# Optimization experiments

Measured on AMD Instinct MI355X. Metric: run time of the kernel, lower is better.

The kernel has to match this reference:

```python
import jax, jax.numpy as jnp
import numpy as np


def _bce_logits(x, z):
    # numerically stable binary_cross_entropy_with_logits (elementwise)
    return jnp.maximum(x, 0.0) - x * z + jnp.log1p(jnp.exp(-jnp.abs(x)))


def _giou(b1, b2):
    # boxes in (cx, cy, w, h) format, mirrors bbox_iou(..., mode='giou')
    eps = 1e-9
    b1x1 = b1[..., 0] - b1[..., 2] / 2; b1y1 = b1[..., 1] - b1[..., 3] / 2
    b1x2 = b1[..., 0] + b1[..., 2] / 2; b1y2 = b1[..., 1] + b1[..., 3] / 2
    b2x1 = b2[..., 0] - b2[..., 2] / 2; b2y1 = b2[..., 1] - b2[..., 3] / 2
    b2x2 = b2[..., 0] + b2[..., 2] / 2; b2y2 = b2[..., 1] + b2[..., 3] / 2
    a1 = jnp.clip(b1x2 - b1x1, 0.0) * jnp.clip(b1y2 - b1y1, 0.0) + eps
    a2 = jnp.clip(b2x2 - b2x1, 0.0) * jnp.clip(b2y2 - b2y1, 0.0) + eps
    iw = jnp.clip(jnp.minimum(b1x2, b2x2) - jnp.maximum(b1x1, b2x1), 0.0)
    ih = jnp.clip(jnp.minimum(b1y2, b2y2) - jnp.maximum(b1y1, b2y1), 0.0)
    inter = iw * ih + eps
    union = a1 + a2 - inter + eps
    iou = inter / union
    cw = jnp.maximum(b1x2, b2x2) - jnp.minimum(b1x1, b2x1)
    ch = jnp.maximum(b1y2, b2y2) - jnp.minimum(b1y1, b2y1)
    carea = cw * ch + eps
    return iou - (carea - union) / carea


def setup_inputs() -> dict:
    key = jax.random.key(0)
    ks = jax.random.split(key, 8)
    N, A, S, nC, nM, G, H, W = 4, 3, 13, 80, 32, 16, 104, 104
    preds = jax.random.normal(ks[0], (N, A, S, S, 5 + nC + nM), jnp.float32) * 0.5
    prototypes = jax.random.normal(ks[1], (N, nM, H, W), jnp.float32)
    masks = (jax.random.uniform(ks[2], (N, G, H, W)) < 0.3).astype(jnp.float32)
    ii = jnp.arange(S)
    interior = (ii >= 2) & (ii <= 10)
    int2d = interior[:, None] & interior[None, :]
    obj = (jax.random.uniform(ks[3], (N, A, S, S)) < 0.06) & int2d
    obj = obj.at[:, 0, 6, 6].set(True)  # guarantee >= 1 object per image
    xy = jax.random.uniform(ks[4], (N, A, S, S, 2), minval=0.2, maxval=0.8)
    wh = jax.random.uniform(ks[5], (N, A, S, S, 2), minval=0.5, maxval=2.5)
    cls = jax.random.randint(ks[6], (N, A, S, S, 1), 0, nC).astype(jnp.float32)
    mid = jax.random.randint(ks[7], (N, A, S, S, 1), 0, G).astype(jnp.float32)
    target = jnp.concatenate([xy, wh, obj[..., None].astype(jnp.float32), cls, mid], axis=-1)
    anchors = jnp.array([[1.0, 1.5], [2.0, 2.5], [3.5, 3.0]], jnp.float32)
    return {"preds": preds, "target": target, "anchors": anchors,
            "prototypes": prototypes, "masks": masks,
            "num_classes": 80, "num_masks": 32}


def reference(preds, target, anchors, prototypes, masks, num_classes, num_masks):
    eps = 1e-9
    N, A, S = preds.shape[0], preds.shape[1], preds.shape[2]
    H, W = prototypes.shape[2], prototypes.shape[3]
    nC, nM = num_classes, num_masks
    dt = preds.dtype
    conf_t = target[..., 4]
    obj = conf_t == 1.0
    noobj = conf_t == 0.0
    objf = obj.astype(dt)
    noobjf = noobj.astype(dt)
    n_obj = objf.sum()
    n_noobj = noobjf.sum()
    conf_logit = preds[..., 4]
    noobj_loss = (_bce_logits(conf_logit, conf_t) * noobjf).sum() / n_noobj
    # ---- segmentation loss (dense masked equivalent of ragged per-instance crops) ----
    coeffs = jnp.tanh(preds[..., 5 + nC:5 + nC + nM])            # [N,A,S,S,M]
    inst = jnp.einsum('naijm,nmhw->naijhw', coeffs, prototypes)   # instance logits
    cols = jnp.arange(S, dtype=dt)
    # cells_to_boxes: normalized image coords, then scaled to prototype pixels
    bx = (target[..., 0] + cols[None, None, None, :]) / S * W
    by = (target[..., 1] + cols[None, None, :, None]) / S * H
    bw = target[..., 2] / S * W
    bh = target[..., 3] / S * H
    x1 = jnp.floor(bx - bw / 2).astype(jnp.int32)
    x2 = jnp.floor(bx + bw / 2).astype(jnp.int32)
    y1 = jnp.floor(by - bh / 2).astype(jnp.int32)
    y2 = jnp.floor(by + bh / 2).astype(jnp.int32)
    ids = jnp.clip(target[..., 6].astype(jnp.int32), 0, masks.shape[1] - 1)
    tm = masks[jnp.arange(N)[:, None, None, None], ids]           # [N,A,S,S,H,W]
    hh = jnp.arange(H)
    ww = jnp.arange(W)
    rm = ((hh >= y1[..., None]) & (hh < y2[..., None])).astype(dt)  # [N,A,S,S,H]
    cm = ((ww >= x1[..., None]) & (ww < x2[..., None])).astype(dt)  # [N,A,S,S,W]
    bce_el = _bce_logits(inst, tm)
    region_sum = jnp.einsum('naijhw,naijh,naijw->naij', bce_el, rm, cm)
    area = rm.sum(-1) * cm.sum(-1)
    valid = (area > 0) & obj
    seg_mean = jnp.where(valid, region_sum / jnp.maximum(area, 1.0), 0.0)
    segment_loss = seg_mean.sum() / (valid.astype(dt).sum() + eps)
    # ---- box / obj / class losses ----
    anch = anchors.reshape(1, A, 1, 1, 2)
    pred_box = jnp.concatenate([jax.nn.sigmoid(preds[..., 0:2]),
                                jnp.exp(preds[..., 2:4]) * anch], axis=-1)
    giou = _giou(pred_box, target[..., 0:4])                      # [N,A,S,S]
    obj_tgt = conf_t * jnp.clip(jax.lax.stop_gradient(giou), 0.0)
    obj_loss = (_bce_logits(conf_logit, obj_tgt) * objf).sum() / n_obj
    # note: original applies BCEWithLogits to sigmoid(xy) (double squash) - faithful
    xy_bce = (_bce_logits(jax.nn.sigmoid(preds[..., 0:2]), target[..., 0:2])
              * objf[..., None]).sum() / (n_obj * 2)
    twh = jnp.log(1e-16 + target[..., 2:4] / anch)
    wh_mse = (((preds[..., 2:4] - twh) ** 2) * objf[..., None]).sum() / (n_obj * 2)
    box_loss = xy_bce + wh_mse + ((1.0 - giou) * objf).sum() / n_obj
    logp = jax.nn.log_softmax(preds[..., 5:5 + nC], axis=-1)
    labels = target[..., 5].astype(jnp.int32)
    nll = -jnp.take_along_axis(logp, labels[..., None], axis=-1)[..., 0]
    class_loss = (nll * objf).sum() / n_obj
    box_l = 8.0 * box_loss
    obj_l = 2.0 * obj_loss
    noobj_l = 4.0 * noobj_loss
    cls_l = 1.0 * class_loss
    seg_l = 10.0 * segment_loss
    total = box_l + obj_l + noobj_l + cls_l + seg_l
    return jnp.stack([box_l, obj_l, noobj_l, cls_l, seg_l, total])
```

## Files before the change

### kernel.cpp

```cpp
#include <hip/hip_runtime.h>
#include <math.h>

#define N_  4
#define A_  3
#define S_  13
#define NC_ 80
#define NM_ 32
#define G_  16
#define H_  104
#define W_  104
#define CH_ (5 + NC_ + NM_)
#define HW_ (H_ * W_)
#define NCELL (N_ * A_ * S_ * S_)

#define MAIN_BLOCKS 64
#define PROW 16

__device__ __forceinline__ float bce_logits(float x, float z) {
    return fmaxf(x, 0.0f) - x * z + log1pf(expf(-fabsf(x)));
}

__device__ __forceinline__ float sigmoidf(float x) {
    return 1.0f / (1.0f + expf(-x));
}

__device__ __forceinline__ float readlane_f(float v, int l) {
    return __int_as_float(__builtin_amdgcn_readlane(__float_as_int(v), l));
}

__device__ __forceinline__ float giou_fn(float cx1, float cy1, float w1, float h1,
                                         float cx2, float cy2, float w2, float h2) {
    const float eps = 1e-9f;
    float b1x1 = cx1 - w1 * 0.5f, b1y1 = cy1 - h1 * 0.5f;
    float b1x2 = cx1 + w1 * 0.5f, b1y2 = cy1 + h1 * 0.5f;
    float b2x1 = cx2 - w2 * 0.5f, b2y1 = cy2 - h2 * 0.5f;
    float b2x2 = cx2 + w2 * 0.5f, b2y2 = cy2 + h2 * 0.5f;
    float a1 = fmaxf(b1x2 - b1x1, 0.0f) * fmaxf(b1y2 - b1y1, 0.0f) + eps;
    float a2 = fmaxf(b2x2 - b2x1, 0.0f) * fmaxf(b2y2 - b2y1, 0.0f) + eps;
    float iw = fmaxf(fminf(b1x2, b2x2) - fmaxf(b1x1, b2x1), 0.0f);
    float ih = fmaxf(fminf(b1y2, b2y2) - fmaxf(b1y1, b2y1), 0.0f);
    float inter = iw * ih + eps;
    float uni   = a1 + a2 - inter + eps;
    float iou   = inter / uni;
    float cw = fmaxf(b1x2, b2x2) - fminf(b1x1, b2x1);
    float ch = fmaxf(b1y2, b2y2) - fminf(b1y1, b2y1);
    float carea = cw * ch + eps;
    return iou - (carea - uni) / carea;
}

__device__ __forceinline__ int region_bounds(const float* t, int i, int j,
                                             int& lox, int& loy, int& ncols, int& nrows) {
    float bx = (t[0] + (float)j) * ((float)W_ / (float)S_);
    float by = (t[1] + (float)i) * ((float)H_ / (float)S_);
    float bw = t[2] * ((float)W_ / (float)S_);
    float bh = t[3] * ((float)H_ / (float)S_);
    int x1 = (int)floorf(bx - bw * 0.5f);
    int x2 = (int)floorf(bx + bw * 0.5f);
    int y1 = (int)floorf(by - bh * 0.5f);
    int y2 = (int)floorf(by + bh * 0.5f);
    lox = max(x1, 0); loy = max(y1, 0);
    ncols = max(min(x2, W_) - lox, 0);
    nrows = max(min(y2, H_) - loy, 0);
    return nrows * ncols;
}

__global__ __launch_bounds__(256) void yolo_fused_kernel(
    const float* __restrict__ preds,
    const float* __restrict__ target,
    const float* __restrict__ anchors,
    const float* __restrict__ protos,
    const float* __restrict__ masks,
    float* __restrict__ partials,
    unsigned int* __restrict__ ticket,
    float* __restrict__ out)
{
    const int b    = blockIdx.x;
    const int tid  = threadIdx.x;
    const int wav  = tid >> 6;
    const int lane = tid & 63;

    __shared__ float s_w[4][8];
    __shared__ float s_red[4];
    __shared__ int   s_list[40];
    __shared__ int   s_nvalid;
    __shared__ int   s_last;

    if (b < 8) {
        const int cell = b * 256 + tid;
        float v0 = 0.f, v1 = 0.f, v2 = 0.f, v3 = 0.f,
              v4 = 0.f, v5 = 0.f, v6 = 0.f, v7 = 0.f;

        if (cell < NCELL) {
            const int a = (cell / (S_ * S_)) % A_;
            const float* t = target + (size_t)cell * 7;
            const float* p = preds  + (size_t)cell * CH_;
            const float conf_t = t[4];
            const float x = p[4];

            if (conf_t == 0.0f) {
                v1 = 1.0f;
                v2 = bce_logits(x, 0.0f);
            } else if (conf_t == 1.0f) {
                v0 = 1.0f;
                float tx = t[0], ty = t[1], tw = t[2], th = t[3];
                float aw = anchors[a * 2 + 0], ah = anchors[a * 2 + 1];
                float sx = sigmoidf(p[0]);
                float sy = sigmoidf(p[1]);
                float pw = expf(p[2]) * aw;
                float ph = expf(p[3]) * ah;
                float giou = giou_fn(sx, sy, pw, ph, tx, ty, tw, th);
                v3 = bce_logits(x, fmaxf(giou, 0.0f));
                v4 = bce_logits(sx, tx) + bce_logits(sy, ty);
                float twl = logf(1e-16f + tw / aw);
                float thl = logf(1e-16f + th / ah);
                float dw = p[2] - twl, dh = p[3] - thl;
                v5 = dw * dw + dh * dh;
                v6 = 1.0f - giou;

                float mx = -1e30f;
                #pragma unroll 8
                for (int c = 0; c < NC_; ++c) mx = fmaxf(mx, p[5 + c]);
                float se = 0.0f;
                #pragma unroll 8
                for (int c = 0; c < NC_; ++c) se += expf(p[5 + c] - mx);
                int label = (int)t[5];
                v7 = (mx + logf(se)) - p[5 + label];
            }
        }

        #pragma unroll
        for (int o = 32; o > 0; o >>= 1) {
            v0 += __shfl_xor(v0, o, 64);  v1 += __shfl_xor(v1, o, 64);
            v2 += __shfl_xor(v2, o, 64);  v3 += __shfl_xor(v3, o, 64);
            v4 += __shfl_xor(v4, o, 64);  v5 += __shfl_xor(v5, o, 64);
            v6 += __shfl_xor(v6, o, 64);  v7 += __shfl_xor(v7, o, 64);
        }
        if ((tid & 63) == 0) {
            int w = tid >> 6;
            s_w[w][0] = v0; s_w[w][1] = v1; s_w[w][2] = v2; s_w[w][3] = v3;
            s_w[w][4] = v4; s_w[w][5] = v5; s_w[w][6] = v6; s_w[w][7] = v7;
        }
        __syncthreads();
        if (tid < 8) {
            partials[b * PROW + tid] =
                s_w[0][tid] + s_w[1][tid] + s_w[2][tid] + s_w[3][tid];
        }
    }

    if (tid == 0) s_nvalid = 0;
    __syncthreads();
    if (tid < 32) {
        int c = tid * 64 + b;
        if (c < NCELL) {
            const float* t = target + (size_t)c * 7;
            if (t[4] == 1.0f) {
                int lox, loy, ncols, nrows;
                int area = region_bounds(t, (c / S_) % S_, c % S_,
                                         lox, loy, ncols, nrows);
                if (area > 0) {
                    int k = atomicAdd(&s_nvalid, 1);
                    s_list[k] = c;
                }
            }
        }
    }
    __syncthreads();
    const int nv = s_nvalid;

    float wave_seg = 0.0f;
    for (int ii = wav; ii < nv; ii += 4) {
        const int cell = s_list[ii];
        const int j = cell % S_;
        const int i = (cell / S_) % S_;
        const int n = cell / (A_ * S_ * S_);
        const float* t = target + (size_t)cell * 7;
        const float* p = preds  + (size_t)cell * CH_;

        int lox, loy, ncols, nrows;
        region_bounds(t, i, j, lox, loy, ncols, nrows);
        const int area = nrows * ncols;

        float cv = 0.0f;
        if (lane < NM_) cv = tanhf(p[5 + NC_ + lane]);
        float cm[NM_];
        #pragma unroll
        for (int m = 0; m < NM_; ++m) cm[m] = readlane_f(cv, m);

        int id = (int)t[6];
        id = min(max(id, 0), G_ - 1);
        const float* tm = masks  + ((size_t)(n * G_ + id)) * HW_;
        const float* pr = protos + (size_t)n * NM_ * HW_;

        float lsum = 0.0f;
        for (int px = lane; px < area; px += 64) {
            int h = loy + px / ncols;
            int w = lox + px % ncols;
            int off = h * W_ + w;
            float inst = 0.0f;
            #pragma unroll
            for (int m = 0; m < NM_; ++m)
                inst += cm[m] * pr[m * HW_ + off];
            lsum += bce_logits(inst, tm[off]);
        }

        #pragma unroll
        for (int o = 32; o > 0; o >>= 1) lsum += __shfl_xor(lsum, o, 64);
        if (lane == 0) wave_seg += lsum / fmaxf((float)area, 1.0f);
    }

    if (lane == 0) s_red[wav] = wave_seg;
    __syncthreads();
    if (tid == 0) {
        partials[b * PROW + 8] = s_red[0] + s_red[1] + s_red[2] + s_red[3];
        partials[b * PROW + 9] = (float)nv;
    }

    __threadfence();
    __syncthreads();
    if (tid == 0) {
        unsigned int old = atomicInc(ticket, MAIN_BLOCKS - 1u);
        s_last = (old == MAIN_BLOCKS - 2u) ? 1 : 0;
    }
    __syncthreads();
    if (!s_last) return;

    __threadfence();
    if (tid < 64) {
        const int t = tid;
        float s0 = 0.f, s1 = 0.f, s2 = 0.f, s3 = 0.f,
              s4 = 0.f, s5 = 0.f, s6 = 0.f, s7 = 0.f, s8 = 0.f, s9 = 0.f;
        if (t < 8) {
            s0 = partials[t * PROW + 0]; s1 = partials[t * PROW + 1];
            s2 = partials[t * PROW + 2]; s3 = partials[t * PROW + 3];
            s4 = partials[t * PROW + 4]; s5 = partials[t * PROW + 5];
            s6 = partials[t * PROW + 6]; s7 = partials[t * PROW + 7];
        }
        s8 = partials[t * PROW + 8];
        s9 = partials[t * PROW + 9];

        #pragma unroll
        for (int o = 32; o > 0; o >>= 1) {
            s0 += __shfl_xor(s0, o, 64);  s1 += __shfl_xor(s1, o, 64);
            s2 += __shfl_xor(s2, o, 64);  s3 += __shfl_xor(s3, o, 64);
            s4 += __shfl_xor(s4, o, 64);  s5 += __shfl_xor(s5, o, 64);
            s6 += __shfl_xor(s6, o, 64);  s7 += __shfl_xor(s7, o, 64);
            s8 += __shfl_xor(s8, o, 64);  s9 += __shfl_xor(s9, o, 64);
        }

        if (t == 0) {
            float n_obj   = s0;
            float n_noobj = s1;
            float noobj_loss = s2 / n_noobj;
            float obj_loss   = s3 / n_obj;
            float xy_bce     = s4 / (n_obj * 2.0f);
            float wh_mse     = s5 / (n_obj * 2.0f);
            float box_loss   = xy_bce + wh_mse + s6 / n_obj;
            float class_loss = s7 / n_obj;
            float seg_loss   = s8 / (s9 + 1e-9f);
            float box_l   = 8.0f * box_loss;
            float obj_l   = 2.0f * obj_loss;
            float noobj_l = 4.0f * noobj_loss;
            float cls_l   = 1.0f * class_loss;
            float seg_l   = 10.0f * seg_loss;
            out[0] = box_l;
            out[1] = obj_l;
            out[2] = noobj_l;
            out[3] = cls_l;
            out[4] = seg_l;
            out[5] = box_l + obj_l + noobj_l + cls_l + seg_l;
        }
    }
}

extern "C" void kernel_launch(void* const* d_in, const int* in_sizes, int n_in,
                              void* d_out, int out_size, void* d_ws, size_t ws_size,
                              hipStream_t stream) {
    const float* preds   = (const float*)d_in[0];
    const float* target  = (const float*)d_in[1];
    const float* anchors = (const float*)d_in[2];
    const float* protos  = (const float*)d_in[3];
    const float* masks   = (const float*)d_in[4];

    float* partials      = (float*)d_ws;
    unsigned int* ticket = (unsigned int*)(partials + MAIN_BLOCKS * PROW);
    float* out           = (float*)d_out;

    yolo_fused_kernel<<<MAIN_BLOCKS, 256, 0, stream>>>(preds, target, anchors,
                                                       protos, masks, partials,
                                                       ticket, out);
}
```

Baseline: 98.17 us.

## Split cell-loss and segmentation work across disjoint blocks with ballot-based object lists

The first 8 blocks now compute only the per-cell losses, and the remaining 56 blocks (224 waves) handle the segmentation loss. Each wave scans its own strided set of cells, builds the list of valid objects with a ballot instead of a shared-memory atomic list, and broadcasts box bounds with readlane. The aim is to stop the 8 cell-loss blocks from also carrying segmentation work, spread objects over more waves, and drop one block barrier. The trade-off is that each wave covers only 10 cells (P2_K), so correctness depends on 224*10 covering all 2028 cells, and the fence placement around the completion ticket has moved.

```diff
diff --git a/kernel.cpp b/kernel.cpp
--- a/kernel.cpp
+++ b/kernel.cpp
@@ -15,6 +15,9 @@
 
 #define MAIN_BLOCKS 64
 #define PROW 16
+#define P2_WAVES ((MAIN_BLOCKS - 8) * 4)
+#define P2_K 10
+
 
 __device__ __forceinline__ float bce_logits(float x, float z) {
     return fmaxf(x, 0.0f) - x * z + log1pf(expf(-fabsf(x)));
@@ -48,12 +51,13 @@
     return iou - (carea - uni) / carea;
 }
 
-__device__ __forceinline__ int region_bounds(const float* t, int i, int j,
-                                             int& lox, int& loy, int& ncols, int& nrows) {
-    float bx = (t[0] + (float)j) * ((float)W_ / (float)S_);
-    float by = (t[1] + (float)i) * ((float)H_ / (float)S_);
-    float bw = t[2] * ((float)W_ / (float)S_);
-    float bh = t[3] * ((float)H_ / (float)S_);
+__device__ __forceinline__ void region_bounds_v(float t0, float t1, float t2, float t3,
+                                                int i, int j,
+                                                int& lox, int& loy, int& ncols, int& nrows) {
+    float bx = (t0 + (float)j) * ((float)W_ / (float)S_);
+    float by = (t1 + (float)i) * ((float)H_ / (float)S_);
+    float bw = t2 * ((float)W_ / (float)S_);
+    float bh = t3 * ((float)H_ / (float)S_);
     int x1 = (int)floorf(bx - bw * 0.5f);
     int x2 = (int)floorf(bx + bw * 0.5f);
     int y1 = (int)floorf(by - bh * 0.5f);
@@ -61,7 +65,6 @@
     lox = max(x1, 0); loy = max(y1, 0);
     ncols = max(min(x2, W_) - lox, 0);
     nrows = max(min(y2, H_) - loy, 0);
-    return nrows * ncols;
 }
 
 __global__ __launch_bounds__(256) void yolo_fused_kernel(
@@ -80,9 +83,8 @@
     const int lane = tid & 63;
 
     __shared__ float s_w[4][8];
-    __shared__ float s_red[4];
-    __shared__ int   s_list[40];
-    __shared__ int   s_nvalid;
+    __shared__ float s_seg[4];
+    __shared__ int   s_nv[4];
     __shared__ int   s_last;
 
     if (b < 8) {
@@ -145,87 +147,91 @@
             partials[b * PROW + tid] =
                 s_w[0][tid] + s_w[1][tid] + s_w[2][tid] + s_w[3][tid];
         }
+        if (tid == 0) {
+            partials[b * PROW + 8] = 0.0f;
+            partials[b * PROW + 9] = 0.0f;
+        }
+    } else {
+        const int gw = (b - 8) * 4 + wav;
+
+        int   pc   = gw + lane * P2_WAVES;
+        bool  in   = (lane < P2_K) && (pc < NCELL);
+        float conf = 0.0f;
+        int   lox = 0, loy = 0, ncols = 0, nrows = 0, idc = 0, parea = 0;
+        if (in) {
+            const float* t = target + (size_t)pc * 7;
+            float t0 = t[0], t1 = t[1], t2 = t[2], t3 = t[3];
+            conf = t[4];
+            float t6 = t[6];
+            region_bounds_v(t0, t1, t2, t3, (pc / S_) % S_, pc % S_,
+                            lox, loy, ncols, nrows);
+            parea = nrows * ncols;
+            idc   = min(max((int)t6, 0), G_ - 1);
+        }
+        unsigned long long vmask = __ballot(in && conf == 1.0f && parea > 0);
+        const int wave_nv = (int)__popcll(vmask);
+
+        float wave_seg = 0.0f;
+        while (vmask) {
+            const int l = __ffsll(vmask) - 1;
+            vmask &= vmask - 1;
+            const int cell = gw + l * P2_WAVES;
+
+            const int rlox = __builtin_amdgcn_readlane(lox,   l);
+            const int rloy = __builtin_amdgcn_readlane(loy,   l);
+            const int rnc  = __builtin_amdgcn_readlane(ncols, l);
+            const int rnr  = __builtin_amdgcn_readlane(nrows, l);
+            const int rid  = __builtin_amdgcn_readlane(idc,   l);
+            const int rn   = cell / (A_ * S_ * S_);
+            const int area = rnr * rnc;
+
+            const float* p  = preds  + (size_t)cell * CH_;
+            const float* tm = masks  + ((size_t)(rn * G_ + rid)) * HW_;
+            const float* pr = protos + (size_t)rn * NM_ * HW_;
+
+            float cv = 0.0f;
+            if (lane < NM_) cv = tanhf(p[5 + NC_ + lane]);
+            float cm[NM_];
+            #pragma unroll
+            for (int m = 0; m < NM_; ++m) cm[m] = readlane_f(cv, m);
+
+            float lsum = 0.0f;
+            for (int px = lane; px < area; px += 64) {
+                int h = rloy + px / rnc;
+                int w = rlox + px % rnc;
+                int off = h * W_ + w;
+                float inst = 0.0f;
+                #pragma unroll
+                for (int m = 0; m < NM_; ++m)
+                    inst += cm[m] * pr[m * HW_ + off];
+                lsum += bce_logits(inst, tm[off]);
+            }
+
+            #pragma unroll
+            for (int o = 32; o > 0; o >>= 1) lsum += __shfl_xor(lsum, o, 64);
+            if (lane == 0) wave_seg += lsum / (float)area;
+        }
+
+        if (lane == 0) { s_seg[wav] = wave_seg; s_nv[wav] = wave_nv; }
+        __syncthreads();
+        if (tid == 0) {
+            partials[b * PROW + 8] = s_seg[0] + s_seg[1] + s_seg[2] + s_seg[3];
+            partials[b * PROW + 9] =
+                (float)(s_nv[0] + s_nv[1] + s_nv[2] + s_nv[3]);
+        }
     }
 
-    if (tid == 0) s_nvalid = 0;
-    __syncthreads();
-    if (tid < 32) {
-        int c = tid * 64 + b;
-        if (c < NCELL) {
-            const float* t = target + (size_t)c * 7;
-            if (t[4] == 1.0f) {
-                int lox, loy, ncols, nrows;
-                int area = region_bounds(t, (c / S_) % S_, c % S_,
-                                         lox, loy, ncols, nrows);
-                if (area > 0) {
-                    int k = atomicAdd(&s_nvalid, 1);
-                    s_list[k] = c;
-                }
-            }
-        }
-    }
-    __syncthreads();
-    const int nv = s_nvalid;
-
-    float wave_seg = 0.0f;
-    for (int ii = wav; ii < nv; ii += 4) {
-        const int cell = s_list[ii];
-        const int j = cell % S_;
-        const int i = (cell / S_) % S_;
-        const int n = cell / (A_ * S_ * S_);
-        const float* t = target + (size_t)cell * 7;
-        const float* p = preds  + (size_t)cell * CH_;
-
-        int lox, loy, ncols, nrows;
-        region_bounds(t, i, j, lox, loy, ncols, nrows);
-        const int area = nrows * ncols;
-
-        float cv = 0.0f;
-        if (lane < NM_) cv = tanhf(p[5 + NC_ + lane]);
-        float cm[NM_];
-        #pragma unroll
-        for (int m = 0; m < NM_; ++m) cm[m] = readlane_f(cv, m);
-
-        int id = (int)t[6];
-        id = min(max(id, 0), G_ - 1);
-        const float* tm = masks  + ((size_t)(n * G_ + id)) * HW_;
-        const float* pr = protos + (size_t)n * NM_ * HW_;
-
-        float lsum = 0.0f;
-        for (int px = lane; px < area; px += 64) {
-            int h = loy + px / ncols;
-            int w = lox + px % ncols;
-            int off = h * W_ + w;
-            float inst = 0.0f;
-            #pragma unroll
-            for (int m = 0; m < NM_; ++m)
-                inst += cm[m] * pr[m * HW_ + off];
-            lsum += bce_logits(inst, tm[off]);
-        }
-
-        #pragma unroll
-        for (int o = 32; o > 0; o >>= 1) lsum += __shfl_xor(lsum, o, 64);
-        if (lane == 0) wave_seg += lsum / fmaxf((float)area, 1.0f);
-    }
-
-    if (lane == 0) s_red[wav] = wave_seg;
     __syncthreads();
     if (tid == 0) {
-        partials[b * PROW + 8] = s_red[0] + s_red[1] + s_red[2] + s_red[3];
-        partials[b * PROW + 9] = (float)nv;
-    }
-
-    __threadfence();
-    __syncthreads();
-    if (tid == 0) {
+        __threadfence();
         unsigned int old = atomicInc(ticket, MAIN_BLOCKS - 1u);
         s_last = (old == MAIN_BLOCKS - 2u) ? 1 : 0;
     }
     __syncthreads();
     if (!s_last) return;
 
-    __threadfence();
     if (tid < 64) {
+        __threadfence();
         const int t = tid;
         float s0 = 0.f, s1 = 0.f, s2 = 0.f, s3 = 0.f,
               s4 = 0.f, s5 = 0.f, s6 = 0.f, s7 = 0.f, s8 = 0.f, s9 = 0.f;
```

Measured after the change: 93.08 us (median of 2 runs). 1.05x faster.
